# Optimization experiments

Measured on AMD Instinct MI355X. Metric: run time of the kernel, lower is better.

Reference implementation:

```python
import jax, jax.numpy as jnp
import numpy as np
import math

D_MODEL = 1024
HEADS = 16
HEAD_DIM = D_MODEL // HEADS
BATCH = 2
SEQ = 2048


def setup_inputs() -> dict:
    key = jax.random.key(0)
    ks = jax.random.split(key, 6)
    scale = 1.0 / math.sqrt(D_MODEL)
    return {
        "x": jax.random.normal(ks[0], (BATCH, SEQ, D_MODEL), dtype=jnp.float32),
        "mask": jnp.zeros((SEQ, SEQ), dtype=jnp.float32),
        "w_qkv": jax.random.normal(ks[1], (D_MODEL, 3 * D_MODEL), dtype=jnp.float32) * scale,
        "b_qkv": jax.random.normal(ks[2], (3 * D_MODEL,), dtype=jnp.float32) * 0.01,
        "w_out": jax.random.normal(ks[3], (D_MODEL, D_MODEL), dtype=jnp.float32) * scale,
        "b_out": jax.random.normal(ks[4], (D_MODEL,), dtype=jnp.float32) * 0.01,
    }


def reference(x, mask, w_qkv, b_qkv, w_out, b_out):
    B, S, D = x.shape
    H, hd = HEADS, HEAD_DIM
    # fused QKV projection: [B,S,3D]
    qkv = x @ w_qkv + b_qkv
    # [B,S,H,3*hd] -> [B,H,S,3*hd]
    qkv = qkv.reshape(B, S, H, 3 * hd).transpose(0, 2, 1, 3)
    q, k, v = jnp.split(qkv, 3, axis=-1)  # each [B,H,S,hd]
    inv_sqrt_d = jnp.asarray(1.0 / math.sqrt(hd), dtype=x.dtype)
    scores = jnp.einsum("bhqd,bhkd->bhqk", q, k) * inv_sqrt_d
    # additive mask; [S,S] broadcasts identically in [H,B,S,S] or [B,H,S,S] layout
    scores = scores + mask
    attn = jax.nn.softmax(scores, axis=-1)
    vals = jnp.einsum("bhqk,bhkd->bhqd", attn, v)  # [B,H,S,hd]
    vals = vals.transpose(0, 2, 1, 3).reshape(B, S, H * hd)
    return vals @ w_out + b_out
```

## Files before the change

### kernel.cpp

```cpp
#include <hip/hip_runtime.h>


typedef __bf16 bf16;
typedef __bf16 bf16x2 __attribute__((ext_vector_type(2)));
typedef __bf16 bf16x4 __attribute__((ext_vector_type(4)));
typedef __bf16 bf16x8 __attribute__((ext_vector_type(8)));
typedef float f32x4 __attribute__((ext_vector_type(4)));

#define MFMA(a, b, c) __builtin_amdgcn_mfma_f32_16x16x32_bf16((a), (b), (c), 0, 0, 0)

#if __has_builtin(__builtin_amdgcn_exp2f)
#define EXP2(x) __builtin_amdgcn_exp2f(x)
#else
#define EXP2(x) exp2f(x)
#endif

__device__ __forceinline__ void load_lds16(const bf16* g, void* l) {
    __builtin_amdgcn_global_load_lds(
        (const __attribute__((address_space(1))) unsigned int*)g,
        (__attribute__((address_space(3))) unsigned int*)l, 16, 0, 0);
}

__global__ void cast4_kernel(const float* __restrict__ in, bf16* __restrict__ out, int n4) {
    int i = blockIdx.x * blockDim.x + threadIdx.x;
    if (i < n4) {
        float4 v = ((const float4*)in)[i];
        bf16x4 o = {(bf16)v.x, (bf16)v.y, (bf16)v.z, (bf16)v.w};
        ((bf16x4*)out)[i] = o;
    }
}

__global__ void transpose_cast_kernel(const float* __restrict__ in, bf16* __restrict__ out,
                                      int R, int C) {
    __shared__ float tile[32][33];
    int bx = blockIdx.x * 32;
    int by = blockIdx.y * 32;
    int tx = threadIdx.x, ty = threadIdx.y;
    for (int i = 0; i < 32; i += 8)
        tile[ty + i][tx] = in[(size_t)(by + ty + i) * C + bx + tx];
    __syncthreads();
    for (int i = 0; i < 32; i += 8)
        out[(size_t)(bx + ty + i) * R + by + tx] = (bf16)tile[tx][ty + i];
}

__global__ __launch_bounds__(256) void gemm_qkv_kernel(
    const bf16* __restrict__ A, const bf16* __restrict__ BT,
    const float* __restrict__ bias,
    bf16* __restrict__ Q, bf16* __restrict__ K, bf16* __restrict__ VT) {
    __shared__ __attribute__((aligned(16))) char lds[2][16384];
    int bm = blockIdx.x, bn = blockIdx.y;
    int t = threadIdx.x;
    int w = t >> 6, lane = t & 63, g = lane >> 4, l16 = lane & 15;
    int wm = (w >> 1) * 64, wn = (w & 1) * 64;
    f32x4 acc[4][4] = {};
    const bf16* Ablk = A + (size_t)(bm * 128) * 1024;
    const bf16* Bblk = BT + (size_t)(bn * 128) * 1024;
    int srow = t >> 2;
    int scg = (t & 3) ^ (srow & 3);
    const bf16* ag0 = Ablk + (size_t)srow * 1024 + scg * 8;
    const bf16* ag1 = ag0 + 64 * 1024;
    const bf16* bg0 = Bblk + (size_t)srow * 1024 + scg * 8;
    const bf16* bg1 = bg0 + 64 * 1024;

    load_lds16(ag0, lds[0] + t * 16);
    load_lds16(ag1, lds[0] + 4096 + t * 16);
    load_lds16(bg0, lds[0] + 8192 + t * 16);
    load_lds16(bg1, lds[0] + 12288 + t * 16);
    asm volatile("s_waitcnt vmcnt(0)" ::: "memory");

    int sw = l16 & 3;
#pragma unroll 2
    for (int j = 0; j < 32; j++) {
        asm volatile("s_barrier" ::: "memory");
        int jp = j + 1 < 32 ? j + 1 : 31;
        char* dst = lds[(j + 1) & 1];
        load_lds16(ag0 + jp * 32, dst + t * 16);
        load_lds16(ag1 + jp * 32, dst + 4096 + t * 16);
        load_lds16(bg0 + jp * 32, dst + 8192 + t * 16);
        load_lds16(bg1 + jp * 32, dst + 12288 + t * 16);

        const bf16* As = (const bf16*)lds[j & 1];
        const bf16* Bs = (const bf16*)(lds[j & 1] + 8192);
        bf16x8 af[4], bfr[4];
#pragma unroll
        for (int mi = 0; mi < 4; mi++) {
            int row = wm + mi * 16 + l16;
            af[mi] = *(const bf16x8*)(&As[row * 32 + (g ^ sw) * 8]);
        }
#pragma unroll
        for (int ni = 0; ni < 4; ni++) {
            int row = wn + ni * 16 + l16;
            bfr[ni] = *(const bf16x8*)(&Bs[row * 32 + (g ^ sw) * 8]);
        }
#pragma unroll
        for (int mi = 0; mi < 4; mi++)
#pragma unroll
            for (int ni = 0; ni < 4; ni++)
                acc[mi][ni] = MFMA(bfr[ni], af[mi], acc[mi][ni]);
        asm volatile("s_waitcnt vmcnt(0)" ::: "memory");
    }
    __syncthreads();

    bf16* vt = (bf16*)lds;
    int b = bm >> 4;
    int row0 = (bm & 15) * 128 + wm;
    int half_col = bn * 128 + wn;
    int h = half_col / 192, tt = half_col % 192;
    size_t bh = (size_t)(b * 16 + h);

    if (tt < 128) {
        bf16* base = (tt == 0 ? Q : K) + bh * 2048 * 64;
#pragma unroll
        for (int mi = 0; mi < 4; mi++) {
#pragma unroll
            for (int ni = 0; ni < 4; ni++) {
                int d0 = ni * 16 + g * 4;
                float4 bv = *(const float4*)(&bias[half_col + d0]);
                int s = row0 + mi * 16 + l16;
                bf16x4 pk = {(bf16)(acc[mi][ni][0] + bv.x), (bf16)(acc[mi][ni][1] + bv.y),
                             (bf16)(acc[mi][ni][2] + bv.z), (bf16)(acc[mi][ni][3] + bv.w)};
                *(bf16x4*)(&base[(size_t)s * 64 + d0]) = pk;
            }
        }
    } else {
#pragma unroll
        for (int mi = 0; mi < 4; mi++) {
            int s_local = wm + mi * 16 + l16;
#pragma unroll
            for (int ni = 0; ni < 4; ni++) {
                int d0 = ni * 16 + g * 4;
                float4 bv = *(const float4*)(&bias[half_col + d0]);
                vt[(d0 + 0) * 136 + s_local] = (bf16)(acc[mi][ni][0] + bv.x);
                vt[(d0 + 1) * 136 + s_local] = (bf16)(acc[mi][ni][1] + bv.y);
                vt[(d0 + 2) * 136 + s_local] = (bf16)(acc[mi][ni][2] + bv.z);
                vt[(d0 + 3) * 136 + s_local] = (bf16)(acc[mi][ni][3] + bv.w);
            }
        }
    }
    __syncthreads();

    int hc0 = bn * 128, hc1 = bn * 128 + 64;
    int vhalf = (hc0 % 192 == 128) ? 0 : ((hc1 % 192 == 128) ? 1 : -1);
    if (vhalf >= 0) {
        int vcol = bn * 128 + vhalf * 64;
        size_t vbh = (size_t)(b * 16 + vcol / 192);
        int d = t >> 2, ch = t & 3;
        const bf16* src = &vt[d * 136 + ch * 32];
        bf16* dstp = &VT[(vbh * 64 + d) * 2048 + (bm & 15) * 128 + ch * 32];
#pragma unroll
        for (int k = 0; k < 2; k++)
            *(bf16x8*)(&dstp[k * 8]) = *(const bf16x8*)(&src[k * 8]);
#pragma unroll
        for (int k = 2; k < 4; k++)
            *(bf16x8*)(&dstp[k * 8]) = *(const bf16x8*)(&src[k * 8]);
    }
}

__global__ __launch_bounds__(256) void gemm_out_kernel(
    const bf16* __restrict__ A, const bf16* __restrict__ BT,
    const float* __restrict__ bias, float* __restrict__ out) {
    __shared__ __attribute__((aligned(16))) char lds[2][12288];
    int bm = blockIdx.x, bn = blockIdx.y;
    int t = threadIdx.x;
    int w = t >> 6, lane = t & 63, g = lane >> 4, l16 = lane & 15;
    int wm = (w >> 1) * 64, wn = (w & 1) * 32;
    f32x4 acc[4][2] = {};
    const bf16* Ablk = A + (size_t)(bm * 128) * 1024;
    const bf16* Bblk = BT + (size_t)(bn * 64) * 1024;
    int srow = t >> 2;
    int scg = (t & 3) ^ (srow & 3);
    const bf16* ag0 = Ablk + (size_t)srow * 1024 + scg * 8;
    const bf16* ag1 = ag0 + 64 * 1024;
    const bf16* bg0 = Bblk + (size_t)srow * 1024 + scg * 8;

    load_lds16(ag0, lds[0] + t * 16);
    load_lds16(ag1, lds[0] + 4096 + t * 16);
    load_lds16(bg0, lds[0] + 8192 + t * 16);
    asm volatile("s_waitcnt vmcnt(0)" ::: "memory");

    int sw = l16 & 3;
#pragma unroll 2
    for (int j = 0; j < 32; j++) {
        asm volatile("s_barrier" ::: "memory");
        int jp = j + 1 < 32 ? j + 1 : 31;
        char* dst = lds[(j + 1) & 1];
        load_lds16(ag0 + jp * 32, dst + t * 16);
        load_lds16(ag1 + jp * 32, dst + 4096 + t * 16);
        load_lds16(bg0 + jp * 32, dst + 8192 + t * 16);

        const bf16* As = (const bf16*)lds[j & 1];
        const bf16* Bs = (const bf16*)(lds[j & 1] + 8192);
        bf16x8 af[4], bfr[2];
#pragma unroll
        for (int mi = 0; mi < 4; mi++) {
            int row = wm + mi * 16 + l16;
            af[mi] = *(const bf16x8*)(&As[row * 32 + (g ^ sw) * 8]);
        }
#pragma unroll
        for (int ni = 0; ni < 2; ni++) {
            int row = wn + ni * 16 + l16;
            bfr[ni] = *(const bf16x8*)(&Bs[row * 32 + (g ^ sw) * 8]);
        }
#pragma unroll
        for (int mi = 0; mi < 4; mi++)
#pragma unroll
            for (int ni = 0; ni < 2; ni++)
                acc[mi][ni] = MFMA(bfr[ni], af[mi], acc[mi][ni]);
        asm volatile("s_waitcnt vmcnt(0)" ::: "memory");
    }

#pragma unroll
    for (int mi = 0; mi < 4; mi++) {
#pragma unroll
        for (int ni = 0; ni < 2; ni++) {
            int row = bm * 128 + wm + mi * 16 + l16;
            int col0 = bn * 64 + wn + ni * 16 + g * 4;
            float4 bv = *(const float4*)(&bias[col0]);
            float4 ov = {acc[mi][ni][0] + bv.x, acc[mi][ni][1] + bv.y,
                         acc[mi][ni][2] + bv.z, acc[mi][ni][3] + bv.w};
            *(float4*)(&out[(size_t)row * 1024 + col0]) = ov;
        }
    }
}

__global__ __launch_bounds__(256, 4) void attn_kernel(
    const bf16* __restrict__ Q, const bf16* __restrict__ K,
    const bf16* __restrict__ VT, const float* __restrict__ mask,
    bf16* __restrict__ vals) {
    __shared__ __attribute__((aligned(16))) char lds[4][8192];

    int blk = blockIdx.x;
    int bh = ((blk & 7) << 2) | ((blk >> 3) & 3);
    int qt = blk >> 5;
    int t = threadIdx.x;
    int w = t >> 6, lane = t & 63, g = lane >> 4, l16 = lane & 15;
    int qw = qt * 64 + w * 16;

    const bf16* Qp = Q + (size_t)bh * 2048 * 64;
    const bf16* Kp = K + (size_t)bh * 2048 * 64;
    const bf16* Vp = VT + (size_t)bh * 64 * 2048;
    const float* mrow = mask + (size_t)(qw + l16) * 2048;

    int ks_row = t >> 3;
    int ks_cblk = (t & 7) ^ (ks_row & 7);
    const bf16* kg = Kp + ks_row * 64 + ks_cblk * 8;
    int vs_d = t >> 2;
    int vs_sblk = (t & 3) ^ ((t >> 3) & 3);
    const bf16* vg = Vp + (size_t)vs_d * 2048 + vs_sblk * 8;

    const float SCL = 0.125f * 1.44269504089f;
    const float L2E = 1.44269504089f;

    bf16x8 q0 = *(const bf16x8*)(&Qp[(size_t)(qw + l16) * 64 + g * 8]);
    bf16x8 q1 = *(const bf16x8*)(&Qp[(size_t)(qw + l16) * 64 + 32 + g * 8]);
    load_lds16(kg + 0, &lds[0][t * 16]);
    load_lds16(vg + 0, &lds[0][4096 + t * 16]);
    float4 mv0 = *(const float4*)(&mrow[0 + g * 4]);
    float4 mv1 = *(const float4*)(&mrow[16 + g * 4]);
    load_lds16(kg + 1 * 32 * 64, &lds[1][t * 16]);
    load_lds16(vg + 1 * 32, &lds[1][4096 + t * 16]);
    asm volatile("s_waitcnt vmcnt(0)" ::: "memory");
    asm volatile("s_barrier" ::: "memory");

    f32x4 o[4] = {};
    float lacc = 0.f;

    for (int j = 0; j < 64; j++) {
        int buf = j & 3;
        int jm = j + 1 < 64 ? j + 1 : 63;
        float4 nmv0 = *(const float4*)(&mrow[jm * 32 + g * 4]);
        float4 nmv1 = *(const float4*)(&mrow[jm * 32 + 16 + g * 4]);
        int jp = j + 2 < 64 ? j + 2 : 63;
        load_lds16(kg + (size_t)jp * 32 * 64, &lds[(j + 2) & 3][t * 16]);
        load_lds16(vg + jp * 32, &lds[(j + 2) & 3][4096 + t * 16]);
        asm volatile("s_waitcnt vmcnt(8)" ::: "memory");
        asm volatile("s_barrier" ::: "memory");

        float p[8];
#pragma unroll
        for (int ts = 0; ts < 2; ts++) {
            int s0 = ts * 16 + l16;
            int swz = s0 & 7;
            bf16x8 k0 = *(const bf16x8*)(&lds[buf][(s0 * 8 + (g ^ swz)) * 16]);
            bf16x8 k1 = *(const bf16x8*)(&lds[buf][(s0 * 8 + ((4 + g) ^ swz)) * 16]);
            f32x4 st = {};
            st = MFMA(k0, q0, st);
            st = MFMA(k1, q1, st);
            float4 mv = ts ? *(float4*)&mv1 : *(float4*)&mv0;
            p[ts * 4 + 0] = EXP2(st[0] * SCL + mv.x * L2E);
            p[ts * 4 + 1] = EXP2(st[1] * SCL + mv.y * L2E);
            p[ts * 4 + 2] = EXP2(st[2] * SCL + mv.z * L2E);
            p[ts * 4 + 3] = EXP2(st[3] * SCL + mv.w * L2E);
        }
#pragma unroll
        for (int i = 0; i < 8; i++) lacc += p[i];

        int dw0, dw1, dw2, dw3;
        { union { bf16x2 h; int i; } u;
          u.h = bf16x2{(bf16)p[0], (bf16)p[1]}; dw0 = u.i;
          u.h = bf16x2{(bf16)p[2], (bf16)p[3]}; dw1 = u.i;
          u.h = bf16x2{(bf16)p[4], (bf16)p[5]}; dw2 = u.i;
          u.h = bf16x2{(bf16)p[6], (bf16)p[7]}; dw3 = u.i; }
        int selA = (((2 * g) & 3) << 4) | l16;
        int selB = (((2 * g + 1) & 3) << 4) | l16;
        int t0a = __shfl(dw0, selA, 64), t2a = __shfl(dw2, selA, 64);
        int t1a = __shfl(dw1, selA, 64), t3a = __shfl(dw3, selA, 64);
        int t0b = __shfl(dw0, selB, 64), t2b = __shfl(dw2, selB, 64);
        int t1b = __shfl(dw1, selB, 64), t3b = __shfl(dw3, selB, 64);
        bool hi = (g & 2) != 0;
        union { int i[4]; bf16x8 v; } pu;
        pu.i[0] = hi ? t2a : t0a;
        pu.i[1] = hi ? t3a : t1a;
        pu.i[2] = hi ? t2b : t0b;
        pu.i[3] = hi ? t3b : t1b;

#pragma unroll
        for (int nc = 0; nc < 4; nc++) {
            int d = nc * 16 + l16;
            int slot = d * 4 + (g ^ ((d >> 1) & 3));
            bf16x8 vf = *(const bf16x8*)(&lds[buf][4096 + slot * 16]);
            o[nc] = MFMA(vf, pu.v, o[nc]);
        }

        mv0 = nmv0;
        mv1 = nmv1;
    }
    asm volatile("s_waitcnt vmcnt(0)" ::: "memory");

    float l = lacc;
    l += __shfl_xor(l, 16, 64);
    l += __shfl_xor(l, 32, 64);
    int b = bh >> 4, h = bh & 15;
    float linv = 1.f / l;
    size_t row = (size_t)(b * 2048 + qw + l16);
#pragma unroll
    for (int nc = 0; nc < 4; nc++) {
        bf16x4 pk = {(bf16)(o[nc][0] * linv), (bf16)(o[nc][1] * linv),
                     (bf16)(o[nc][2] * linv), (bf16)(o[nc][3] * linv)};
        *(bf16x4*)(&vals[row * 1024 + h * 64 + nc * 16 + g * 4]) = pk;
    }
}

extern "C" void kernel_launch(void* const* d_in, const int* in_sizes, int n_in,
                              void* d_out, int out_size, void* d_ws, size_t ws_size,
                              hipStream_t stream) {
    const float* x     = (const float*)d_in[0];
    const float* mask  = (const float*)d_in[1];
    const float* w_qkv = (const float*)d_in[2];
    const float* b_qkv = (const float*)d_in[3];
    const float* w_out = (const float*)d_in[4];
    const float* b_out = (const float*)d_in[5];
    float* out = (float*)d_out;

    char* ws = (char*)d_ws;
    size_t off = 0;
    bf16* xb    = (bf16*)(ws + off); off += (size_t)4096 * 1024 * 2;
    bf16* wqkvT = (bf16*)(ws + off); off += (size_t)3072 * 1024 * 2;
    bf16* woutT = (bf16*)(ws + off); off += (size_t)1024 * 1024 * 2;
    bf16* Qa    = (bf16*)(ws + off); off += (size_t)32 * 2048 * 64 * 2;
    bf16* Ka    = (bf16*)(ws + off); off += (size_t)32 * 2048 * 64 * 2;
    bf16* VTa   = (bf16*)(ws + off); off += (size_t)32 * 64 * 2048 * 2;
    bf16* vals  = (bf16*)(ws + off); off += (size_t)4096 * 1024 * 2;

    cast4_kernel<<<4096, 256, 0, stream>>>(x, xb, 4096 * 1024 / 4);
    transpose_cast_kernel<<<dim3(96, 32), dim3(32, 8), 0, stream>>>(w_qkv, wqkvT, 1024, 3072);
    transpose_cast_kernel<<<dim3(32, 32), dim3(32, 8), 0, stream>>>(w_out, woutT, 1024, 1024);
    gemm_qkv_kernel<<<dim3(32, 24), 256, 0, stream>>>(xb, wqkvT, b_qkv, Qa, Ka, VTa);
    attn_kernel<<<1024, 256, 0, stream>>>(Qa, Ka, VTa, mask, vals);
    gemm_out_kernel<<<dim3(32, 16), 256, 0, stream>>>(vals, woutT, b_out, out);
}
```

Before: 239.3 us.

## Process two 16-row query tiles per wave in attention kernel

Each wave now handles 32 query rows instead of 16, reusing each K and V fragment read from LDS for two MFMA chains. This halves the grid to 512 blocks and halves the per-query-row K/V global-to-LDS traffic and barrier count. In exchange it doubles accumulators and mask loads per wave, relaxes the launch-bounds occupancy hint from 4 to 2, and adjusts the vmcnt wait for the extra mask loads. It also merges two split copy loops in the QKV epilogue with no behavioural effect.

Result: faster. 232.8 us (-2.7%).

```diff
diff --git a/kernel.cpp b/kernel.cpp
--- a/kernel.cpp
+++ b/kernel.cpp
@@ -148,10 +148,7 @@
         const bf16* src = &vt[d * 136 + ch * 32];
         bf16* dstp = &VT[(vbh * 64 + d) * 2048 + (bm & 15) * 128 + ch * 32];
 #pragma unroll
-        for (int k = 0; k < 2; k++)
-            *(bf16x8*)(&dstp[k * 8]) = *(const bf16x8*)(&src[k * 8]);
-#pragma unroll
-        for (int k = 2; k < 4; k++)
+        for (int k = 0; k < 4; k++)
             *(bf16x8*)(&dstp[k * 8]) = *(const bf16x8*)(&src[k * 8]);
     }
 }
@@ -223,7 +220,7 @@
     }
 }
 
-__global__ __launch_bounds__(256, 4) void attn_kernel(
+__global__ __launch_bounds__(256, 2) void attn_kernel(
     const bf16* __restrict__ Q, const bf16* __restrict__ K,
     const bf16* __restrict__ VT, const float* __restrict__ mask,
     bf16* __restrict__ vals) {
@@ -234,12 +231,13 @@
     int qt = blk >> 5;
     int t = threadIdx.x;
     int w = t >> 6, lane = t & 63, g = lane >> 4, l16 = lane & 15;
-    int qw = qt * 64 + w * 16;
+    int qw = qt * 128 + w * 32;
 
     const bf16* Qp = Q + (size_t)bh * 2048 * 64;
     const bf16* Kp = K + (size_t)bh * 2048 * 64;
     const bf16* Vp = VT + (size_t)bh * 64 * 2048;
-    const float* mrow = mask + (size_t)(qw + l16) * 2048;
+    const float* mrowA = mask + (size_t)(qw + l16) * 2048;
+    const float* mrowB = mask + (size_t)(qw + 16 + l16) * 2048;
 
     int ks_row = t >> 3;
     int ks_cblk = (t & 7) ^ (ks_row & 7);
@@ -251,93 +249,130 @@
     const float SCL = 0.125f * 1.44269504089f;
     const float L2E = 1.44269504089f;
 
-    bf16x8 q0 = *(const bf16x8*)(&Qp[(size_t)(qw + l16) * 64 + g * 8]);
-    bf16x8 q1 = *(const bf16x8*)(&Qp[(size_t)(qw + l16) * 64 + 32 + g * 8]);
+    bf16x8 qa0 = *(const bf16x8*)(&Qp[(size_t)(qw + l16) * 64 + g * 8]);
+    bf16x8 qa1 = *(const bf16x8*)(&Qp[(size_t)(qw + l16) * 64 + 32 + g * 8]);
+    bf16x8 qb0 = *(const bf16x8*)(&Qp[(size_t)(qw + 16 + l16) * 64 + g * 8]);
+    bf16x8 qb1 = *(const bf16x8*)(&Qp[(size_t)(qw + 16 + l16) * 64 + 32 + g * 8]);
     load_lds16(kg + 0, &lds[0][t * 16]);
     load_lds16(vg + 0, &lds[0][4096 + t * 16]);
-    float4 mv0 = *(const float4*)(&mrow[0 + g * 4]);
-    float4 mv1 = *(const float4*)(&mrow[16 + g * 4]);
+    float4 mva0 = *(const float4*)(&mrowA[0 + g * 4]);
+    float4 mva1 = *(const float4*)(&mrowA[16 + g * 4]);
+    float4 mvb0 = *(const float4*)(&mrowB[0 + g * 4]);
+    float4 mvb1 = *(const float4*)(&mrowB[16 + g * 4]);
     load_lds16(kg + 1 * 32 * 64, &lds[1][t * 16]);
     load_lds16(vg + 1 * 32, &lds[1][4096 + t * 16]);
     asm volatile("s_waitcnt vmcnt(0)" ::: "memory");
     asm volatile("s_barrier" ::: "memory");
 
-    f32x4 o[4] = {};
-    float lacc = 0.f;
+    f32x4 o[4][2] = {};
+    float la = 0.f, lb = 0.f;
 
     for (int j = 0; j < 64; j++) {
         int buf = j & 3;
         int jm = j + 1 < 64 ? j + 1 : 63;
-        float4 nmv0 = *(const float4*)(&mrow[jm * 32 + g * 4]);
-        float4 nmv1 = *(const float4*)(&mrow[jm * 32 + 16 + g * 4]);
+        float4 nmva0 = *(const float4*)(&mrowA[jm * 32 + g * 4]);
+        float4 nmva1 = *(const float4*)(&mrowA[jm * 32 + 16 + g * 4]);
+        float4 nmvb0 = *(const float4*)(&mrowB[jm * 32 + g * 4]);
+        float4 nmvb1 = *(const float4*)(&mrowB[jm * 32 + 16 + g * 4]);
         int jp = j + 2 < 64 ? j + 2 : 63;
         load_lds16(kg + (size_t)jp * 32 * 64, &lds[(j + 2) & 3][t * 16]);
         load_lds16(vg + jp * 32, &lds[(j + 2) & 3][4096 + t * 16]);
-        asm volatile("s_waitcnt vmcnt(8)" ::: "memory");
+        asm volatile("s_waitcnt vmcnt(12)" ::: "memory");
         asm volatile("s_barrier" ::: "memory");
 
-        float p[8];
+        float pa[8], pb[8];
 #pragma unroll
         for (int ts = 0; ts < 2; ts++) {
             int s0 = ts * 16 + l16;
             int swz = s0 & 7;
             bf16x8 k0 = *(const bf16x8*)(&lds[buf][(s0 * 8 + (g ^ swz)) * 16]);
             bf16x8 k1 = *(const bf16x8*)(&lds[buf][(s0 * 8 + ((4 + g) ^ swz)) * 16]);
-            f32x4 st = {};
-            st = MFMA(k0, q0, st);
-            st = MFMA(k1, q1, st);
-            float4 mv = ts ? *(float4*)&mv1 : *(float4*)&mv0;
-            p[ts * 4 + 0] = EXP2(st[0] * SCL + mv.x * L2E);
-            p[ts * 4 + 1] = EXP2(st[1] * SCL + mv.y * L2E);
-            p[ts * 4 + 2] = EXP2(st[2] * SCL + mv.z * L2E);
-            p[ts * 4 + 3] = EXP2(st[3] * SCL + mv.w * L2E);
-        }
-#pragma unroll
-        for (int i = 0; i < 8; i++) lacc += p[i];
-
-        int dw0, dw1, dw2, dw3;
-        { union { bf16x2 h; int i; } u;
-          u.h = bf16x2{(bf16)p[0], (bf16)p[1]}; dw0 = u.i;
-          u.h = bf16x2{(bf16)p[2], (bf16)p[3]}; dw1 = u.i;
-          u.h = bf16x2{(bf16)p[4], (bf16)p[5]}; dw2 = u.i;
-          u.h = bf16x2{(bf16)p[6], (bf16)p[7]}; dw3 = u.i; }
+            f32x4 sta = {}, stb = {};
+            sta = MFMA(k0, qa0, sta);
+            sta = MFMA(k1, qa1, sta);
+            stb = MFMA(k0, qb0, stb);
+            stb = MFMA(k1, qb1, stb);
+            float4 ma = ts ? mva1 : mva0;
+            float4 mb = ts ? mvb1 : mvb0;
+            pa[ts * 4 + 0] = EXP2(sta[0] * SCL + ma.x * L2E);
+            pa[ts * 4 + 1] = EXP2(sta[1] * SCL + ma.y * L2E);
+            pa[ts * 4 + 2] = EXP2(sta[2] * SCL + ma.z * L2E);
+            pa[ts * 4 + 3] = EXP2(sta[3] * SCL + ma.w * L2E);
+            pb[ts * 4 + 0] = EXP2(stb[0] * SCL + mb.x * L2E);
+            pb[ts * 4 + 1] = EXP2(stb[1] * SCL + mb.y * L2E);
+            pb[ts * 4 + 2] = EXP2(stb[2] * SCL + mb.z * L2E);
+            pb[ts * 4 + 3] = EXP2(stb[3] * SCL + mb.w * L2E);
+        }
+#pragma unroll
+        for (int i = 0; i < 8; i++) { la += pa[i]; lb += pb[i]; }
+
         int selA = (((2 * g) & 3) << 4) | l16;
         int selB = (((2 * g + 1) & 3) << 4) | l16;
-        int t0a = __shfl(dw0, selA, 64), t2a = __shfl(dw2, selA, 64);
-        int t1a = __shfl(dw1, selA, 64), t3a = __shfl(dw3, selA, 64);
-        int t0b = __shfl(dw0, selB, 64), t2b = __shfl(dw2, selB, 64);
-        int t1b = __shfl(dw1, selB, 64), t3b = __shfl(dw3, selB, 64);
         bool hi = (g & 2) != 0;
-        union { int i[4]; bf16x8 v; } pu;
-        pu.i[0] = hi ? t2a : t0a;
-        pu.i[1] = hi ? t3a : t1a;
-        pu.i[2] = hi ? t2b : t0b;
-        pu.i[3] = hi ? t3b : t1b;
+        union { int i[4]; bf16x8 v; } pua, pub;
+        {
+            union { bf16x2 h; int i; } u;
+            int dw0, dw1, dw2, dw3;
+            u.h = bf16x2{(bf16)pa[0], (bf16)pa[1]}; dw0 = u.i;
+            u.h = bf16x2{(bf16)pa[2], (bf16)pa[3]}; dw1 = u.i;
+            u.h = bf16x2{(bf16)pa[4], (bf16)pa[5]}; dw2 = u.i;
+            u.h = bf16x2{(bf16)pa[6], (bf16)pa[7]}; dw3 = u.i;
+            int t0a = __shfl(dw0, selA, 64), t2a = __shfl(dw2, selA, 64);
+            int t1a = __shfl(dw1, selA, 64), t3a = __shfl(dw3, selA, 64);
+            int t0b = __shfl(dw0, selB, 64), t2b = __shfl(dw2, selB, 64);
+            int t1b = __shfl(dw1, selB, 64), t3b = __shfl(dw3, selB, 64);
+            pua.i[0] = hi ? t2a : t0a;
+            pua.i[1] = hi ? t3a : t1a;
+            pua.i[2] = hi ? t2b : t0b;
+            pua.i[3] = hi ? t3b : t1b;
+        }
+        {
+            union { bf16x2 h; int i; } u;
+            int dw0, dw1, dw2, dw3;
+            u.h = bf16x2{(bf16)pb[0], (bf16)pb[1]}; dw0 = u.i;
+            u.h = bf16x2{(bf16)pb[2], (bf16)pb[3]}; dw1 = u.i;
+            u.h = bf16x2{(bf16)pb[4], (bf16)pb[5]}; dw2 = u.i;
+            u.h = bf16x2{(bf16)pb[6], (bf16)pb[7]}; dw3 = u.i;
+            int t0a = __shfl(dw0, selA, 64), t2a = __shfl(dw2, selA, 64);
+            int t1a = __shfl(dw1, selA, 64), t3a = __shfl(dw3, selA, 64);
+            int t0b = __shfl(dw0, selB, 64), t2b = __shfl(dw2, selB, 64);
+            int t1b = __shfl(dw1, selB, 64), t3b = __shfl(dw3, selB, 64);
+            pub.i[0] = hi ? t2a : t0a;
+            pub.i[1] = hi ? t3a : t1a;
+            pub.i[2] = hi ? t2b : t0b;
+            pub.i[3] = hi ? t3b : t1b;
+        }
 
 #pragma unroll
         for (int nc = 0; nc < 4; nc++) {
             int d = nc * 16 + l16;
             int slot = d * 4 + (g ^ ((d >> 1) & 3));
             bf16x8 vf = *(const bf16x8*)(&lds[buf][4096 + slot * 16]);
-            o[nc] = MFMA(vf, pu.v, o[nc]);
-        }
-
-        mv0 = nmv0;
-        mv1 = nmv1;
+            o[nc][0] = MFMA(vf, pua.v, o[nc][0]);
+            o[nc][1] = MFMA(vf, pub.v, o[nc][1]);
+        }
+
+        mva0 = nmva0; mva1 = nmva1;
+        mvb0 = nmvb0; mvb1 = nmvb1;
     }
     asm volatile("s_waitcnt vmcnt(0)" ::: "memory");
 
-    float l = lacc;
-    l += __shfl_xor(l, 16, 64);
-    l += __shfl_xor(l, 32, 64);
+    la += __shfl_xor(la, 16, 64);
+    la += __shfl_xor(la, 32, 64);
+    lb += __shfl_xor(lb, 16, 64);
+    lb += __shfl_xor(lb, 32, 64);
     int b = bh >> 4, h = bh & 15;
-    float linv = 1.f / l;
-    size_t row = (size_t)(b * 2048 + qw + l16);
+    float lia = 1.f / la, lib = 1.f / lb;
+    size_t rowA = (size_t)(b * 2048 + qw + l16);
+    size_t rowB = rowA + 16;
 #pragma unroll
     for (int nc = 0; nc < 4; nc++) {
-        bf16x4 pk = {(bf16)(o[nc][0] * linv), (bf16)(o[nc][1] * linv),
-                     (bf16)(o[nc][2] * linv), (bf16)(o[nc][3] * linv)};
-        *(bf16x4*)(&vals[row * 1024 + h * 64 + nc * 16 + g * 4]) = pk;
+        bf16x4 pkA = {(bf16)(o[nc][0][0] * lia), (bf16)(o[nc][0][1] * lia),
+                      (bf16)(o[nc][0][2] * lia), (bf16)(o[nc][0][3] * lia)};
+        *(bf16x4*)(&vals[rowA * 1024 + h * 64 + nc * 16 + g * 4]) = pkA;
+        bf16x4 pkB = {(bf16)(o[nc][1][0] * lib), (bf16)(o[nc][1][1] * lib),
+                      (bf16)(o[nc][1][2] * lib), (bf16)(o[nc][1][3] * lib)};
+        *(bf16x4*)(&vals[rowB * 1024 + h * 64 + nc * 16 + g * 4]) = pkB;
     }
 }
 
@@ -366,6 +401,6 @@
     transpose_cast_kernel<<<dim3(96, 32), dim3(32, 8), 0, stream>>>(w_qkv, wqkvT, 1024, 3072);
     transpose_cast_kernel<<<dim3(32, 32), dim3(32, 8), 0, stream>>>(w_out, woutT, 1024, 1024);
     gemm_qkv_kernel<<<dim3(32, 24), 256, 0, stream>>>(xb, wqkvT, b_qkv, Qa, Ka, VTa);
-    attn_kernel<<<1024, 256, 0, stream>>>(Qa, Ka, VTa, mask, vals);
+    attn_kernel<<<512, 256, 0, stream>>>(Qa, Ka, VTa, mask, vals);
     gemm_out_kernel<<<dim3(32, 16), 256, 0, stream>>>(vals, woutT, b_out, out);
 }
```
